# Performance work log

Measured on AMD Instinct MI355X. Metric: run time of the kernel, lower is better.

## Reference

```python
import jax, jax.numpy as jnp
import numpy as np
from jax import lax


def setup_inputs() -> dict:
    key = jax.random.key(0)
    k1, k2, k3, k4, k5 = jax.random.split(key, 5)
    B, C_in, H, W = 32768, 3, 14, 14
    C_out, kh, kw = 16, 5, 5
    num_outputs = 1000
    return {
        "feature_map": jax.random.normal(k1, (B, C_in, H, W), dtype=jnp.float32),
        "conv_w": jax.random.normal(k2, (C_out, C_in, kh, kw), dtype=jnp.float32),
        "conv_b": jax.random.normal(k3, (C_out,), dtype=jnp.float32),
        "lin_w": jax.random.normal(k4, (num_outputs, C_out * 5 * 5), dtype=jnp.float32),
        "lin_b": jax.random.normal(k5, (num_outputs,), dtype=jnp.float32),
    }


def reference(feature_map, conv_w, conv_b, lin_w, lin_b):
    # Conv2D: valid cross-correlation, stride 1, no padding (B,Ci,H,W)x(Co,Ci,h,w)->(B,Co,H-h+1,W-w+1)
    y = lax.conv_general_dilated(
        feature_map, conv_w, window_strides=(1, 1), padding="VALID",
        dimension_numbers=("NCHW", "OIHW", "NCHW"))
    y = jax.nn.relu(y + conv_b[None, :, None, None])
    # Non-overlapping 2x2 max pool: (B,C,10,10) -> (B,C,5,5)
    B, C, H, W = y.shape
    y = y.reshape(B, C, H // 2, 2, W // 2, 2).max(axis=(3, 5))
    # Linear head on flattened features (B, C*5*5) -> (B, num_outputs)
    out = y.reshape(B, -1) @ lin_w.T + lin_b
    return out
```

## Files before the change

kernel.cpp:

```cpp
#include <hip/hip_runtime.h>
#include <stdint.h>

#define BTOT 32768
#define NIMG 16
#define KF   416

typedef __attribute__((ext_vector_type(2))) _Float16 half2r;
typedef __attribute__((ext_vector_type(8))) short short8;
typedef __attribute__((ext_vector_type(4))) float floatx4;

static __device__ __forceinline__ half2r u2h(unsigned int u) {
    return __builtin_bit_cast(half2r, u);
}
static __device__ __forceinline__ unsigned int h2u(half2r h) {
    return __builtin_bit_cast(unsigned int, h);
}
static __device__ __forceinline__ half2r cvt2h(float a, float b) {
    return __builtin_bit_cast(half2r, __builtin_amdgcn_cvt_pkrtz(a, b));
}
__device__ __forceinline__ unsigned short f2bf(float x) {
    union { float f; unsigned int u; } v; v.f = x;
    unsigned int r = v.u + 0x7fffu + ((v.u >> 16) & 1u);
    return (unsigned short)(r >> 16);
}

__global__ __launch_bounds__(256) void conv_pool_kernel(
    const float* __restrict__ fm, const float* __restrict__ cw,
    const float* __restrict__ cb, unsigned short* __restrict__ feat)
{
    __shared__ __align__(16) unsigned int s_img[NIMG * 294];
    __shared__ unsigned int s_w2[16 * 76];

    const int tid = threadIdx.x;
    const int b0 = blockIdx.x * NIMG;

    const float4* in4 = (const float4*)fm;
    for (int idx = tid; idx < NIMG * 147; idx += 256) {
        float4 v = in4[(size_t)b0 * 147 + idx];
        half2r lo = cvt2h(v.x, v.y);
        half2r hi = cvt2h(v.z, v.w);
        *(uint2*)&s_img[idx * 2] = make_uint2(h2u(lo), h2u(hi));
    }
    for (int idx = tid; idx < 1200; idx += 256) {
        int co = idx / 75;
        int r = idx - co * 75;
        float w = cw[idx];
        s_w2[co * 76 + r] = h2u(cvt2h(w, w));
    }
    __syncthreads();

    const int b_local = tid & 15;
    const int co = tid >> 4;
    const float bias = cb[co];
    const unsigned int* ibase = s_img + b_local * 294;
    const unsigned int* wbase = s_w2 + co * 76;
    unsigned short* fout = feat + (size_t)(b0 + b_local) * KF + co * 25;

    for (int r = 0; r < 5; ++r) {
        half2r acc0[5], acc1[5];
        #pragma unroll
        for (int p = 0; p < 5; ++p) { acc0[p] = u2h(0u); acc1[p] = u2h(0u); }

        #pragma unroll
        for (int ci = 0; ci < 3; ++ci) {
            const unsigned int* ip = ibase + ci * 98 + r * 14;
            unsigned int wr[25];
            #pragma unroll
            for (int k = 0; k < 25; ++k) wr[k] = wbase[ci * 25 + k];

            #pragma unroll
            for (int ir = 0; ir < 6; ++ir) {
                unsigned int v[7];
                #pragma unroll
                for (int q = 0; q < 7; ++q) v[q] = ip[ir * 7 + q];
                unsigned int s[6];
                #pragma unroll
                for (int q = 0; q < 6; ++q) s[q] = (v[q] >> 16) | (v[q + 1] << 16);

                if (ir < 5) {
                    #pragma unroll
                    for (int p = 0; p < 5; ++p) {
                        acc0[p] += u2h(v[p])     * u2h(wr[ir * 5 + 0]);
                        acc0[p] += u2h(s[p])     * u2h(wr[ir * 5 + 1]);
                        acc0[p] += u2h(v[p + 1]) * u2h(wr[ir * 5 + 2]);
                        acc0[p] += u2h(s[p + 1]) * u2h(wr[ir * 5 + 3]);
                        acc0[p] += u2h(v[p + 2]) * u2h(wr[ir * 5 + 4]);
                    }
                }
                if (ir >= 1) {
                    const int kh = ir - 1;
                    #pragma unroll
                    for (int p = 0; p < 5; ++p) {
                        acc1[p] += u2h(v[p])     * u2h(wr[kh * 5 + 0]);
                        acc1[p] += u2h(s[p])     * u2h(wr[kh * 5 + 1]);
                        acc1[p] += u2h(v[p + 1]) * u2h(wr[kh * 5 + 2]);
                        acc1[p] += u2h(s[p + 1]) * u2h(wr[kh * 5 + 3]);
                        acc1[p] += u2h(v[p + 2]) * u2h(wr[kh * 5 + 4]);
                    }
                }
            }
        }
        #pragma unroll
        for (int p = 0; p < 5; ++p) {
            float a = (float)acc0[p].x, b = (float)acc0[p].y;
            float c = (float)acc1[p].x, d = (float)acc1[p].y;
            float m = fmaxf(fmaxf(a, b), fmaxf(c, d)) + bias;
            m = fmaxf(m, 0.f);
            fout[r * 5 + p] = f2bf(m);
        }
    }
    if (co == 0) {
        uint4 z = make_uint4(0u, 0u, 0u, 0u);
        *(uint4*)(feat + (size_t)(b0 + b_local) * KF + 400) = z;
        *(uint4*)(feat + (size_t)(b0 + b_local) * KF + 408) = z;
    }
}

__global__ __launch_bounds__(256) void prep_w_kernel(const float* __restrict__ lw,
                                                     unsigned short* __restrict__ Wb)
{
    int c = blockIdx.x * 256 + threadIdx.x;
    if (c >= 1024 * 52) return;
    int n = c / 52;
    int kc = (c - n * 52) * 8;
    unsigned short v[8];
    #pragma unroll
    for (int j = 0; j < 8; ++j) {
        int k = kc + j;
        float x = (n < 1000 && k < 400) ? lw[n * 400 + k] : 0.f;
        v[j] = f2bf(x);
    }
    *(uint4*)(Wb + (size_t)n * KF + kc) = *(uint4*)v;
}

__global__ __launch_bounds__(256) void gemm_kernel(
    const unsigned short* __restrict__ F, const unsigned short* __restrict__ Wb,
    const float* __restrict__ lb, float* __restrict__ out)
{
    __shared__ __align__(16) unsigned short At[128 * 32];
    __shared__ __align__(16) unsigned short Bt[128 * 32];

    const int tid = threadIdx.x;
    const int bm = blockIdx.x >> 3;
    const int bn = blockIdx.x & 7;
    const int m0 = bm * 128;
    const int n0 = bn * 128;

    const int w = tid >> 6;
    const int lane = tid & 63;
    const int wm = w & 1, wn = w >> 1;
    const int lq = lane >> 4, ln = lane & 15;

    floatx4 zero = {0.f, 0.f, 0.f, 0.f};
    floatx4 acc[4][4];
    #pragma unroll
    for (int i = 0; i < 4; ++i)
        #pragma unroll
        for (int j = 0; j < 4; ++j) acc[i][j] = zero;

    const int srow = w * 16 + (lane >> 2);
    const int skc = (lane & 3) * 8;
    const unsigned short* gA = F + (size_t)(m0 + srow) * KF + skc;
    const unsigned short* gB = Wb + (size_t)(n0 + srow) * KF + skc;

    for (int kb = 0; kb < KF; kb += 32) {
        #pragma unroll
        for (int t = 0; t < 2; ++t) {
            __builtin_amdgcn_global_load_lds(
                (const __attribute__((address_space(1))) void*)(gA + (size_t)(t * 64) * KF + kb),
                (__attribute__((address_space(3))) void*)&At[(w * 16 + t * 64) * 32],
                16, 0, 0);
            __builtin_amdgcn_global_load_lds(
                (const __attribute__((address_space(1))) void*)(gB + (size_t)(t * 64) * KF + kb),
                (__attribute__((address_space(3))) void*)&Bt[(w * 16 + t * 64) * 32],
                16, 0, 0);
        }
        __syncthreads();
        short8 af[4], bf[4];
        #pragma unroll
        for (int i = 0; i < 4; ++i)
            af[i] = *(const short8*)&At[(wm * 64 + i * 16 + ln) * 32 + lq * 8];
        #pragma unroll
        for (int j = 0; j < 4; ++j)
            bf[j] = *(const short8*)&Bt[(wn * 64 + j * 16 + ln) * 32 + lq * 8];
        #pragma unroll
        for (int i = 0; i < 4; ++i)
            #pragma unroll
            for (int j = 0; j < 4; ++j)
                acc[i][j] = __builtin_amdgcn_mfma_f32_16x16x32_bf16(af[i], bf[j], acc[i][j], 0, 0, 0);
        __syncthreads();
    }

    #pragma unroll
    for (int j = 0; j < 4; ++j) {
        int n = n0 + wn * 64 + j * 16 + ln;
        if (n >= 1000) continue;
        float bias = lb[n];
        #pragma unroll
        for (int i = 0; i < 4; ++i) {
            int mb = m0 + wm * 64 + i * 16 + lq * 4;
            #pragma unroll
            for (int rr = 0; rr < 4; ++rr)
                out[(size_t)(mb + rr) * 1000 + n] = acc[i][j][rr] + bias;
        }
    }
}

extern "C" void kernel_launch(void* const* d_in, const int* in_sizes, int n_in,
                              void* d_out, int out_size, void* d_ws, size_t ws_size,
                              hipStream_t stream)
{
    const float* fm = (const float*)d_in[0];
    const float* cw = (const float*)d_in[1];
    const float* cb = (const float*)d_in[2];
    const float* lw = (const float*)d_in[3];
    const float* lb = (const float*)d_in[4];
    float* out = (float*)d_out;

    unsigned short* feat = (unsigned short*)d_ws;
    unsigned short* Wb   = (unsigned short*)d_ws + (size_t)BTOT * KF;

    prep_w_kernel<<<208, 256, 0, stream>>>(lw, Wb);
    conv_pool_kernel<<<BTOT / NIMG, 256, 0, stream>>>(fm, cw, cb, feat);
    gemm_kernel<<<2048, 256, 0, stream>>>(feat, Wb, lb, out);
}
```

Before: 339.3 us.

## Restructure GEMM to stage weight slab in LDS and stream A from global

The GEMM now uses 512-thread blocks. Each block loads a 128-column weight slab into LDS in two K-halves, while each wave reads its 64 A rows directly from global memory into registers, with a one-step prefetch. Each wave computes a 64x128 tile. This removes the per-K-step LDS staging of A and the barriers around it, and amortizes the B load over 512 rows. The cost is more registers per thread (128 accumulator floats) and uncoalesced-ish direct global A reads.

Result: slower. 347.7 us (+2.4%).

```diff
diff --git a/kernel.cpp b/kernel.cpp
--- a/kernel.cpp
+++ b/kernel.cpp
@@ -133,72 +133,86 @@
     *(uint4*)(Wb + (size_t)n * KF + kc) = *(uint4*)v;
 }
 
-__global__ __launch_bounds__(256) void gemm_kernel(
+#define H0C 28
+#define H1C 24
+
+__global__ __launch_bounds__(512, 2) void gemm_kernel(
     const unsigned short* __restrict__ F, const unsigned short* __restrict__ Wb,
     const float* __restrict__ lb, float* __restrict__ out)
 {
-    __shared__ __align__(16) unsigned short At[128 * 32];
-    __shared__ __align__(16) unsigned short Bt[128 * 32];
+    __shared__ __align__(16) unsigned short Bs[H0C * 128 * 8];
 
     const int tid = threadIdx.x;
-    const int bm = blockIdx.x >> 3;
-    const int bn = blockIdx.x & 7;
-    const int m0 = bm * 128;
-    const int n0 = bn * 128;
-
+    const int lane = tid & 63;
     const int w = tid >> 6;
-    const int lane = tid & 63;
-    const int wm = w & 1, wn = w >> 1;
     const int lq = lane >> 4, ln = lane & 15;
 
+    const int slab = blockIdx.x & 7;
+    const int mg = blockIdx.x >> 3;
+    const int n0 = slab * 128;
+    const int mbase = mg * 512 + w * 64;
+
     floatx4 zero = {0.f, 0.f, 0.f, 0.f};
-    floatx4 acc[4][4];
+    floatx4 acc[4][8];
     #pragma unroll
     for (int i = 0; i < 4; ++i)
         #pragma unroll
-        for (int j = 0; j < 4; ++j) acc[i][j] = zero;
-
-    const int srow = w * 16 + (lane >> 2);
-    const int skc = (lane & 3) * 8;
-    const unsigned short* gA = F + (size_t)(m0 + srow) * KF + skc;
-    const unsigned short* gB = Wb + (size_t)(n0 + srow) * KF + skc;
-
-    for (int kb = 0; kb < KF; kb += 32) {
-        #pragma unroll
-        for (int t = 0; t < 2; ++t) {
-            __builtin_amdgcn_global_load_lds(
-                (const __attribute__((address_space(1))) void*)(gA + (size_t)(t * 64) * KF + kb),
-                (__attribute__((address_space(3))) void*)&At[(w * 16 + t * 64) * 32],
-                16, 0, 0);
-            __builtin_amdgcn_global_load_lds(
-                (const __attribute__((address_space(1))) void*)(gB + (size_t)(t * 64) * KF + kb),
-                (__attribute__((address_space(3))) void*)&Bt[(w * 16 + t * 64) * 32],
-                16, 0, 0);
+        for (int j = 0; j < 8; ++j) acc[i][j] = zero;
+
+    const unsigned short* Arow = F + (size_t)(mbase + ln) * KF + lq * 8;
+
+    #pragma unroll
+    for (int half = 0; half < 2; ++half) {
+        const int c0 = half ? H0C : 0;
+        const int nch = half ? H1C : H0C;
+        for (int idx = tid; idx < nch * 128; idx += 512) {
+            int c = idx >> 7;
+            int n = idx & 127;
+            uint4 v = *(const uint4*)&Wb[(size_t)(n0 + n) * KF + (c0 + c) * 8];
+            *(uint4*)&Bs[(c * 128 + n) * 8] = v;
         }
         __syncthreads();
-        short8 af[4], bf[4];
+
+        const int kbeg = c0 * 8;
+        const int kend = kbeg + nch * 8;
+
+        short8 af[4], afn[4];
         #pragma unroll
         for (int i = 0; i < 4; ++i)
-            af[i] = *(const short8*)&At[(wm * 64 + i * 16 + ln) * 32 + lq * 8];
-        #pragma unroll
-        for (int j = 0; j < 4; ++j)
-            bf[j] = *(const short8*)&Bt[(wn * 64 + j * 16 + ln) * 32 + lq * 8];
-        #pragma unroll
-        for (int i = 0; i < 4; ++i)
-            #pragma unroll
-            for (int j = 0; j < 4; ++j)
-                acc[i][j] = __builtin_amdgcn_mfma_f32_16x16x32_bf16(af[i], bf[j], acc[i][j], 0, 0, 0);
+            af[i] = *(const short8*)(Arow + (size_t)(i * 16) * KF + kbeg);
+
+        for (int kb = kbeg; kb < kend; kb += 32) {
+            int kbn = (kb + 32 < kend) ? kb + 32 : kb;
+            #pragma unroll
+            for (int i = 0; i < 4; ++i)
+                afn[i] = *(const short8*)(Arow + (size_t)(i * 16) * KF + kbn);
+
+            const int cl = ((kb - kbeg) >> 3) + lq;
+            short8 bf[8];
+            #pragma unroll
+            for (int j = 0; j < 8; ++j)
+                bf[j] = *(const short8*)&Bs[(cl * 128 + j * 16 + ln) * 8];
+
+            #pragma unroll
+            for (int i = 0; i < 4; ++i)
+                #pragma unroll
+                for (int j = 0; j < 8; ++j)
+                    acc[i][j] = __builtin_amdgcn_mfma_f32_16x16x32_bf16(af[i], bf[j], acc[i][j], 0, 0, 0);
+
+            #pragma unroll
+            for (int i = 0; i < 4; ++i) af[i] = afn[i];
+        }
         __syncthreads();
     }
 
     #pragma unroll
-    for (int j = 0; j < 4; ++j) {
-        int n = n0 + wn * 64 + j * 16 + ln;
+    for (int j = 0; j < 8; ++j) {
+        int n = n0 + j * 16 + ln;
         if (n >= 1000) continue;
         float bias = lb[n];
         #pragma unroll
         for (int i = 0; i < 4; ++i) {
-            int mb = m0 + wm * 64 + i * 16 + lq * 4;
+            int mb = mbase + i * 16 + lq * 4;
             #pragma unroll
             for (int rr = 0; rr < 4; ++rr)
                 out[(size_t)(mb + rr) * 1000 + n] = acc[i][j][rr] + bias;
@@ -222,5 +236,5 @@
 
     prep_w_kernel<<<208, 256, 0, stream>>>(lw, Wb);
     conv_pool_kernel<<<BTOT / NIMG, 256, 0, stream>>>(fm, cw, cb, feat);
-    gemm_kernel<<<2048, 256, 0, stream>>>(feat, Wb, lb, out);
-}
+    gemm_kernel<<<512, 512, 0, stream>>>(feat, Wb, lb, out);
+}
```
